# Kernel tuning notes

Hardware: AMD Instinct MI355X
Metric: run time of the kernel (lower is better)

The kernel has to match this reference:

```python
import jax, jax.numpy as jnp
import numpy as np

VQ_ALPHA = 0.5   # non-trainable vq_alpha weight, constant 0.5
BETA = 0.25      # commitment loss weight


def setup_inputs() -> dict:
    key = jax.random.key(0)
    k1, k2 = jax.random.split(key)
    x = jax.random.normal(k1, (16, 64, 64, 256), dtype=jnp.float32)
    # tf.keras RandomUniform default is U(-0.05, 0.05)
    dictionary = jax.random.uniform(k2, (256, 1024), dtype=jnp.float32,
                                    minval=-0.05, maxval=0.05)
    return {"x": x, "dictionary": dictionary}


def reference(x, dictionary):
    D, K = dictionary.shape  # embedding_dim, num_embeddings
    flat = x.reshape(-1, D)  # [N, D]

    # squared L2 distances: ||f||^2 + ||d||^2 - 2 f.d   -> [N, K]
    similarity = flat @ dictionary
    distances = (jnp.sum(flat * flat, axis=1, keepdims=True)
                 + jnp.sum(dictionary * dictionary, axis=0, keepdims=True)
                 - 2.0 * similarity)
    code_idx = jnp.argmin(distances, axis=1)  # [N]

    # one-hot @ dict^T is just a row gather of dict^T
    quantized = jnp.take(dictionary.T, code_idx, axis=0)  # [N, D]
    quantized = VQ_ALPHA * quantized
    q = quantized.reshape(x.shape)

    dictionary_loss = jnp.mean(jnp.square(jax.lax.stop_gradient(x) - q))
    commitment_loss = jnp.mean(jnp.square(x - jax.lax.stop_gradient(q)))
    loss = dictionary_loss + BETA * commitment_loss

    # straight-through estimator
    q_st = x + jax.lax.stop_gradient(q - x)
    return q_st, loss
```

## Files before the change

### kernel.cpp

```cpp
#include <hip/hip_runtime.h>


#define NROWS   65536
#define DIM     256
#define NCODE   1024
#define RPB     64
#define EPS_TIE 4e-3f

typedef _Float16 half8 __attribute__((ext_vector_type(8)));
typedef float    f32x4 __attribute__((ext_vector_type(4)));


__global__ void k_transpose(const float* __restrict__ dict, float* __restrict__ dictT) {
    int t = blockIdx.x * 256 + threadIdx.x;
#pragma unroll
    for (int i = 0; i < 4; ++i) {
        int e = i * 65536 + t;
        int d = e >> 10, k = e & 1023;
        dictT[k * DIM + d] = dict[e];
    }
}

__global__ void k_norms(const float* __restrict__ dict, float* __restrict__ dictnorm) {
    int k = blockIdx.x * 256 + threadIdx.x;
    float s = 0.f;
#pragma unroll 8
    for (int d = 0; d < DIM; ++d) {
        float v = dict[d * NCODE + k];
        s = fmaf(v, v, s);
    }
    dictnorm[k] = s;
}

__global__ void k_pack(const float* __restrict__ dict, unsigned short* __restrict__ packB) {
    int gid = blockIdx.x * 256 + threadIdx.x;
#pragma unroll
    for (int ii = 0; ii < 4; ++ii) {
        int o = ii * 65536 + gid;
        int j = o & 7, q = (o >> 3) & 3, n = (o >> 5) & 1023, kk = o >> 15;
        int d = kk * 32 + q * 8 + j;
        _Float16 h = (_Float16)dict[d * NCODE + n];
        packB[o] = *(unsigned short*)&h;
    }
}

__device__ __forceinline__ float np_pairwise_sq_128(const float* a, int stride) {
    float r[8];
#pragma unroll
    for (int j = 0; j < 8; ++j) {
        float v = a[j * stride];
        r[j] = __fmul_rn(v, v);
    }
    for (int i = 8; i < 128; i += 8) {
#pragma unroll
        for (int j = 0; j < 8; ++j) {
            float v = a[(i + j) * stride];
            r[j] = __fadd_rn(r[j], __fmul_rn(v, v));
        }
    }
    return __fadd_rn(__fadd_rn(__fadd_rn(r[0], r[1]), __fadd_rn(r[2], r[3])),
                     __fadd_rn(__fadd_rn(r[4], r[5]), __fadd_rn(r[6], r[7])));
}


__global__ __launch_bounds__(256, 4) void k_vq(
    const float* __restrict__ x, const float* __restrict__ dict,
    const float* __restrict__ dictT, const float* __restrict__ dictnorm,
    const unsigned short* __restrict__ packB,
    float* __restrict__ out, double* __restrict__ block_sums)
{
    __shared__ __align__(16) unsigned short bstage[8 * 2048];
    __shared__ float row_m1[RPB], row_m2[RPB];
    __shared__ int   row_k1[RPB], row_k2[RPB];
    __shared__ float red_d[256];
    __shared__ int   red_k[256];
    __shared__ float wred[4];
    __shared__ int   amb_list[RPB];
    __shared__ int   amb_cnt;

    const int tid  = threadIdx.x;
    const int ln   = tid & 63, wv = tid >> 6;
    const int l15  = ln & 15, q = ln >> 4;
    const int row0 = blockIdx.x * RPB;

    if (tid == 0) amb_cnt = 0;

    half8 afrag[8];
    {
        const float* ar = x + (size_t)(row0 + wv * 16 + l15) * DIM + q * 8;
#pragma unroll
        for (int kk = 0; kk < 8; ++kk) {
            const float4 p0 = *(const float4*)(ar + kk * 32);
            const float4 p1 = *(const float4*)(ar + kk * 32 + 4);
            half8 h;
            h[0] = (_Float16)p0.x; h[1] = (_Float16)p0.y; h[2] = (_Float16)p0.z; h[3] = (_Float16)p0.w;
            h[4] = (_Float16)p1.x; h[5] = (_Float16)p1.y; h[6] = (_Float16)p1.z; h[7] = (_Float16)p1.w;
            afrag[kk] = h;
        }
    }

    float m1[4], m2[4]; int j1[4], j2[4];
#pragma unroll
    for (int i = 0; i < 4; ++i) { m1[i] = 3.0e38f; m2[i] = 3.0e38f; j1[i] = 0x7fffffff; j2[i] = 0x7fffffff; }

    for (int cc = 0; cc < 16; ++cc) {
        const int c0 = cc * 64;
        __syncthreads();
        {
            const unsigned short* src = packB + (size_t)c0 * 32 + tid * 8;
            uint4 tmp[8];
#pragma unroll
            for (int kk = 0; kk < 8; ++kk) tmp[kk] = *(const uint4*)(src + (size_t)kk * 32768);
#pragma unroll
            for (int kk = 0; kk < 8; ++kk) *(uint4*)&bstage[kk * 2048 + tid * 8] = tmp[kk];
        }
        __syncthreads();

        float dn[4];
#pragma unroll
        for (int t = 0; t < 4; ++t) dn[t] = dictnorm[c0 + t * 16 + l15];

        const f32x4 zero = {0.f, 0.f, 0.f, 0.f};
        f32x4 acc[4];
#pragma unroll
        for (int t = 0; t < 4; ++t) acc[t] = zero;

#pragma unroll
        for (int kk = 0; kk < 8; ++kk) {
#pragma unroll
            for (int t = 0; t < 4; ++t) {
                const half8 b = *(const half8*)&bstage[kk * 2048 + (t * 16 + l15) * 32 + q * 8];
                acc[t] = __builtin_amdgcn_mfma_f32_16x16x32_f16(afrag[kk], b, acc[t], 0, 0, 0);
            }
        }

#pragma unroll
        for (int t = 0; t < 4; ++t) {
            const int k = c0 + t * 16 + l15;
#pragma unroll
            for (int i = 0; i < 4; ++i) {
                const float s = fmaf(-2.f, acc[t][i], dn[t]);
                if (s < m1[i])      { m2[i] = m1[i]; j2[i] = j1[i]; m1[i] = s; j1[i] = k; }
                else if (s < m2[i]) { m2[i] = s; j2[i] = k; }
            }
        }
    }

#pragma unroll
    for (int i = 0; i < 4; ++i) {
        float a1 = m1[i], a2 = m2[i]; int b1 = j1[i], b2 = j2[i];
#pragma unroll
        for (int sft = 1; sft < 16; sft <<= 1) {
            float o1 = __shfl_xor(a1, sft);
            float o2 = __shfl_xor(a2, sft);
            int   p1 = __shfl_xor(b1, sft);
            int   p2 = __shfl_xor(b2, sft);
            if (o1 < a1 || (o1 == a1 && p1 < b1)) {
                bool t = (a1 < o2) || (a1 == o2 && b1 < p2);
                a2 = t ? a1 : o2; b2 = t ? b1 : p2;
                a1 = o1; b1 = p1;
            } else {
                bool t = (o1 < a2) || (o1 == a2 && p1 < b2);
                a2 = t ? o1 : a2; b2 = t ? p1 : b2;
            }
        }
        if (l15 == 0) {
            const int r = wv * 16 + q * 4 + i;
            row_m1[r] = a1; row_m2[r] = a2; row_k1[r] = b1; row_k2[r] = b2;
        }
    }
    __syncthreads();

    if (tid < RPB && (row_m2[tid] - row_m1[tid]) < EPS_TIE) {
        int p = atomicAdd(&amb_cnt, 1);
        amb_list[p] = tid;
    }
    __syncthreads();
    const int namb = amb_cnt;

    for (int a = 0; a < namb; ++a) {
        const int r = amb_list[a];
        const float* xr = x + (size_t)(row0 + r) * DIM;
        const float nf = __fadd_rn(np_pairwise_sq_128(xr, 1), np_pairwise_sq_128(xr + 128, 1));
        float bd = 3.4e38f; int bk = 0x7fffffff;
#pragma unroll
        for (int i = 0; i < 4; ++i) {
            const int k = i * 256 + tid;
            float sim = 0.f, nd = 0.f;
            for (int d = 0; d < DIM; ++d) {
                const float dv = dict[(size_t)d * NCODE + k];
                const float fv = xr[d];
                sim = fmaf(fv, dv, sim);
                nd  = __fadd_rn(nd, __fmul_rn(dv, dv));
            }
            const float dist = __fsub_rn(__fadd_rn(nf, nd), __fmul_rn(2.f, sim));
            if (dist < bd) { bd = dist; bk = k; }
        }
        red_d[tid] = bd; red_k[tid] = bk;
        __syncthreads();
        for (int s = 128; s > 0; s >>= 1) {
            if (tid < s) {
                const float od = red_d[tid + s]; const int ok = red_k[tid + s];
                if (od < red_d[tid] || (od == red_d[tid] && ok < red_k[tid])) {
                    red_d[tid] = od; red_k[tid] = ok;
                }
            }
            __syncthreads();
        }
        if (tid == 0) row_k1[r] = red_k[0];
        __syncthreads();
    }

    float lsum = 0.f;
#pragma unroll 2
    for (int i = 0; i < 16; ++i) {
        const int e = i * 1024 + tid * 4;
        const int r = e >> 8, d0 = e & 255;
        const int kk = row_k1[r];
        const float4 dv = *(const float4*)&dictT[(size_t)kk * DIM + d0];
        const float4 xv = *(const float4*)&x[(size_t)row0 * DIM + e];
        float4 qv; qv.x = 0.5f * dv.x; qv.y = 0.5f * dv.y; qv.z = 0.5f * dv.z; qv.w = 0.5f * dv.w;
        float4 ov;
        ov.x = __fadd_rn(xv.x, __fsub_rn(qv.x, xv.x));
        ov.y = __fadd_rn(xv.y, __fsub_rn(qv.y, xv.y));
        ov.z = __fadd_rn(xv.z, __fsub_rn(qv.z, xv.z));
        ov.w = __fadd_rn(xv.w, __fsub_rn(qv.w, xv.w));
        const float e0 = __fsub_rn(xv.x, qv.x), e1 = __fsub_rn(xv.y, qv.y);
        const float e2 = __fsub_rn(xv.z, qv.z), e3 = __fsub_rn(xv.w, qv.w);
        lsum += e0 * e0 + e1 * e1 + e2 * e2 + e3 * e3;
        *(float4*)&out[(size_t)row0 * DIM + e] = ov;
    }

#pragma unroll
    for (int sft = 32; sft > 0; sft >>= 1) lsum += __shfl_down(lsum, sft, 64);
    if ((tid & 63) == 0) wred[tid >> 6] = lsum;
    __syncthreads();
    if (tid == 0)
        block_sums[blockIdx.x] = (double)((wred[0] + wred[1]) + (wred[2] + wred[3]));
}


__global__ void k_finalize(const double* __restrict__ block_sums, float* __restrict__ out_loss) {
    __shared__ double w[16];
    const int t = threadIdx.x;
    double v = block_sums[t];
#pragma unroll
    for (int sft = 32; sft > 0; sft >>= 1) v += __shfl_down(v, sft, 64);
    if ((t & 63) == 0) w[t >> 6] = v;
    __syncthreads();
    if (t == 0) {
        double tot = 0.0;
        for (int i = 0; i < 16; ++i) tot += w[i];
        out_loss[0] = (float)(1.25 * tot / (double)(NROWS * DIM));
    }
}


extern "C" void kernel_launch(void* const* d_in, const int* in_sizes, int n_in,
                              void* d_out, int out_size, void* d_ws, size_t ws_size,
                              hipStream_t stream) {
    (void)in_sizes; (void)n_in; (void)out_size; (void)ws_size;
    const float* x    = (const float*)d_in[0];
    const float* dict = (const float*)d_in[1];
    float* out = (float*)d_out;

    char* ws = (char*)d_ws;
    float*          dictT      = (float*)ws;
    float*          dictnorm   = (float*)(ws + 1048576);
    double*         block_sums = (double*)(ws + 1048576 + 4096);
    unsigned short* packB      = (unsigned short*)(ws + 1048576 + 4096 + 8192);

    k_transpose<<<256, 256, 0, stream>>>(dict, dictT);
    k_norms<<<4, 256, 0, stream>>>(dict, dictnorm);
    k_pack<<<256, 256, 0, stream>>>(dict, packB);
    k_vq<<<NROWS / RPB, 256, 0, stream>>>(x, dict, dictT, dictnorm, packB, out, block_sums);
    k_finalize<<<1, 1024, 0, stream>>>(block_sums, out + (size_t)NROWS * DIM);
}
```

Before: 305.8 us.

## Double-buffer codebook via async LDS loads, 128 rows per block, packed argmin

Merges the three dictionary prep kernels into one and doubles rows per block to 128, so each wave computes two 16-row MFMA tiles that share every B fragment loaded from LDS. Codebook tiles are staged with global_load_lds into a double buffer, letting the next chunk load while the current one is multiplied, which removes one barrier per chunk. The top-2 tracking packs a truncated distance and the code index into one unsigned key, so the running min and the shuffle reduction become integer min/max. The distance offset of +8 keeps the keys positive so integer ordering matches float ordering. The cost is a wider tie threshold to absorb the truncation, higher register and LDS use, and occupancy reduced to 2 blocks per CU.

```diff
diff --git a/kernel.cpp b/kernel.cpp
--- a/kernel.cpp
+++ b/kernel.cpp
@@ -4,43 +4,34 @@
 #define NROWS   65536
 #define DIM     256
 #define NCODE   1024
-#define RPB     64
-#define EPS_TIE 4e-3f
+#define RPB     128
+#define NBLK    (NROWS / RPB)
+#define EPS_TIE 6e-3f
 
 typedef _Float16 half8 __attribute__((ext_vector_type(8)));
 typedef float    f32x4 __attribute__((ext_vector_type(4)));
 
-
-__global__ void k_transpose(const float* __restrict__ dict, float* __restrict__ dictT) {
-    int t = blockIdx.x * 256 + threadIdx.x;
-#pragma unroll
-    for (int i = 0; i < 4; ++i) {
-        int e = i * 65536 + t;
-        int d = e >> 10, k = e & 1023;
-        dictT[k * DIM + d] = dict[e];
-    }
-}
-
-__global__ void k_norms(const float* __restrict__ dict, float* __restrict__ dictnorm) {
-    int k = blockIdx.x * 256 + threadIdx.x;
-    float s = 0.f;
-#pragma unroll 8
-    for (int d = 0; d < DIM; ++d) {
-        float v = dict[d * NCODE + k];
-        s = fmaf(v, v, s);
-    }
-    dictnorm[k] = s;
-}
-
-__global__ void k_pack(const float* __restrict__ dict, unsigned short* __restrict__ packB) {
+__global__ void k_prep(const float* __restrict__ dict, float* __restrict__ dictT,
+                       float* __restrict__ dictnorm, unsigned short* __restrict__ packB) {
     int gid = blockIdx.x * 256 + threadIdx.x;
 #pragma unroll
     for (int ii = 0; ii < 4; ++ii) {
         int o = ii * 65536 + gid;
-        int j = o & 7, q = (o >> 3) & 3, n = (o >> 5) & 1023, kk = o >> 15;
-        int d = kk * 32 + q * 8 + j;
-        _Float16 h = (_Float16)dict[d * NCODE + n];
-        packB[o] = *(unsigned short*)&h;
+        { int d = o >> 10, k = o & 1023; dictT[k * DIM + d] = dict[o]; }
+        { int j = o & 7, q = (o >> 3) & 3, n = (o >> 5) & 1023, kk = o >> 15;
+          int d = kk * 32 + q * 8 + j;
+          _Float16 h = (_Float16)dict[d * NCODE + n];
+          packB[o] = *(unsigned short*)&h; }
+    }
+    if (blockIdx.x < 4) {
+        int k = blockIdx.x * 256 + threadIdx.x;
+        float s = 0.f;
+#pragma unroll 8
+        for (int d = 0; d < DIM; ++d) {
+            float v = dict[d * NCODE + k];
+            s = fmaf(v, v, s);
+        }
+        dictnorm[k] = s + 8.0f;
     }
 }
 
@@ -63,15 +54,28 @@
 }
 
 
-__global__ __launch_bounds__(256, 4) void k_vq(
+#define STAGE(buf, cc) do {                                                            \
+    const int _t = tid >> 6, _q = (tid >> 4) & 3, _n = tid & 15;                       \
+    const unsigned short* _s = packB + (size_t)(cc) * 2048                             \
+                             + ((_t * 16 + _n) * 32 + _q * 8);                         \
+    unsigned short* _d = &bstage[buf][tid * 8];                                        \
+    _Pragma("unroll")                                                                  \
+    for (int _k = 0; _k < 8; ++_k)                                                     \
+        __builtin_amdgcn_global_load_lds(                                              \
+            (const __attribute__((address_space(1))) unsigned int*)(_s + (size_t)_k * 32768), \
+            (__attribute__((address_space(3))) unsigned int*)(_d + _k * 2048),         \
+            16, 0, 0);                                                                 \
+} while (0)
+
+__global__ __launch_bounds__(256, 2) void k_vq(
     const float* __restrict__ x, const float* __restrict__ dict,
     const float* __restrict__ dictT, const float* __restrict__ dictnorm,
     const unsigned short* __restrict__ packB,
     float* __restrict__ out, double* __restrict__ block_sums)
 {
-    __shared__ __align__(16) unsigned short bstage[8 * 2048];
-    __shared__ float row_m1[RPB], row_m2[RPB];
-    __shared__ int   row_k1[RPB], row_k2[RPB];
+    __shared__ __align__(16) unsigned short bstage[2][8 * 2048];
+    __shared__ float row_gap[RPB];
+    __shared__ int   row_k1[RPB];
     __shared__ float red_d[256];
     __shared__ int   red_k[256];
     __shared__ float wred[4];
@@ -82,12 +86,15 @@
     const int ln   = tid & 63, wv = tid >> 6;
     const int l15  = ln & 15, q = ln >> 4;
     const int row0 = blockIdx.x * RPB;
-
+    const int wrow = row0 + wv * 32;
+
+    STAGE(0, 0);
     if (tid == 0) amb_cnt = 0;
 
-    half8 afrag[8];
-    {
-        const float* ar = x + (size_t)(row0 + wv * 16 + l15) * DIM + q * 8;
+    half8 afrag[2][8];
+#pragma unroll
+    for (int u = 0; u < 2; ++u) {
+        const float* ar = x + (size_t)(wrow + u * 16 + l15) * DIM + q * 8;
 #pragma unroll
         for (int kk = 0; kk < 8; ++kk) {
             const float4 p0 = *(const float4*)(ar + kk * 32);
@@ -95,83 +102,84 @@
             half8 h;
             h[0] = (_Float16)p0.x; h[1] = (_Float16)p0.y; h[2] = (_Float16)p0.z; h[3] = (_Float16)p0.w;
             h[4] = (_Float16)p1.x; h[5] = (_Float16)p1.y; h[6] = (_Float16)p1.z; h[7] = (_Float16)p1.w;
-            afrag[kk] = h;
-        }
-    }
-
-    float m1[4], m2[4]; int j1[4], j2[4];
-#pragma unroll
-    for (int i = 0; i < 4; ++i) { m1[i] = 3.0e38f; m2[i] = 3.0e38f; j1[i] = 0x7fffffff; j2[i] = 0x7fffffff; }
+            afrag[u][kk] = h;
+        }
+    }
+
+    unsigned p1v[2][4], p2v[2][4];
+#pragma unroll
+    for (int u = 0; u < 2; ++u)
+#pragma unroll
+        for (int i = 0; i < 4; ++i) { p1v[u][i] = 0xFFFFFFFFu; p2v[u][i] = 0xFFFFFFFFu; }
+
+    __syncthreads();
 
     for (int cc = 0; cc < 16; ++cc) {
+        const int cur = cc & 1;
+        if (cc < 15) STAGE(cur ^ 1, cc + 1);
+
         const int c0 = cc * 64;
+        float dn[4];
+#pragma unroll
+        for (int t = 0; t < 4; ++t) dn[t] = dictnorm[c0 + t * 16 + l15];
+
+        const f32x4 zero = {0.f, 0.f, 0.f, 0.f};
+        f32x4 acc[2][4];
+#pragma unroll
+        for (int u = 0; u < 2; ++u)
+#pragma unroll
+            for (int t = 0; t < 4; ++t) acc[u][t] = zero;
+
+#pragma unroll
+        for (int kk = 0; kk < 8; ++kk) {
+#pragma unroll
+            for (int t = 0; t < 4; ++t) {
+                const half8 b = *(const half8*)&bstage[cur][kk * 2048 + t * 512 + ln * 8];
+                acc[0][t] = __builtin_amdgcn_mfma_f32_16x16x32_f16(afrag[0][kk], b, acc[0][t], 0, 0, 0);
+                acc[1][t] = __builtin_amdgcn_mfma_f32_16x16x32_f16(afrag[1][kk], b, acc[1][t], 0, 0, 0);
+            }
+        }
+
+#pragma unroll
+        for (int t = 0; t < 4; ++t) {
+            const unsigned kbase = (unsigned)(c0 + t * 16 + l15);
+#pragma unroll
+            for (int u = 0; u < 2; ++u)
+#pragma unroll
+                for (int i = 0; i < 4; ++i) {
+                    const float s = fmaf(-2.f, acc[u][t][i], dn[t]);
+                    const unsigned pk = (__float_as_uint(s) & 0xFFFFFC00u) | kbase;
+                    const unsigned mx = p1v[u][i] > pk ? p1v[u][i] : pk;
+                    p2v[u][i] = p2v[u][i] < mx ? p2v[u][i] : mx;
+                    p1v[u][i] = p1v[u][i] < pk ? p1v[u][i] : pk;
+                }
+        }
         __syncthreads();
-        {
-            const unsigned short* src = packB + (size_t)c0 * 32 + tid * 8;
-            uint4 tmp[8];
-#pragma unroll
-            for (int kk = 0; kk < 8; ++kk) tmp[kk] = *(const uint4*)(src + (size_t)kk * 32768);
-#pragma unroll
-            for (int kk = 0; kk < 8; ++kk) *(uint4*)&bstage[kk * 2048 + tid * 8] = tmp[kk];
-        }
-        __syncthreads();
-
-        float dn[4];
-#pragma unroll
-        for (int t = 0; t < 4; ++t) dn[t] = dictnorm[c0 + t * 16 + l15];
-
-        const f32x4 zero = {0.f, 0.f, 0.f, 0.f};
-        f32x4 acc[4];
-#pragma unroll
-        for (int t = 0; t < 4; ++t) acc[t] = zero;
-
-#pragma unroll
-        for (int kk = 0; kk < 8; ++kk) {
-#pragma unroll
-            for (int t = 0; t < 4; ++t) {
-                const half8 b = *(const half8*)&bstage[kk * 2048 + (t * 16 + l15) * 32 + q * 8];
-                acc[t] = __builtin_amdgcn_mfma_f32_16x16x32_f16(afrag[kk], b, acc[t], 0, 0, 0);
-            }
-        }
-
-#pragma unroll
-        for (int t = 0; t < 4; ++t) {
-            const int k = c0 + t * 16 + l15;
-#pragma unroll
-            for (int i = 0; i < 4; ++i) {
-                const float s = fmaf(-2.f, acc[t][i], dn[t]);
-                if (s < m1[i])      { m2[i] = m1[i]; j2[i] = j1[i]; m1[i] = s; j1[i] = k; }
-                else if (s < m2[i]) { m2[i] = s; j2[i] = k; }
-            }
-        }
-    }
-
-#pragma unroll
-    for (int i = 0; i < 4; ++i) {
-        float a1 = m1[i], a2 = m2[i]; int b1 = j1[i], b2 = j2[i];
-#pragma unroll
-        for (int sft = 1; sft < 16; sft <<= 1) {
-            float o1 = __shfl_xor(a1, sft);
-            float o2 = __shfl_xor(a2, sft);
-            int   p1 = __shfl_xor(b1, sft);
-            int   p2 = __shfl_xor(b2, sft);
-            if (o1 < a1 || (o1 == a1 && p1 < b1)) {
-                bool t = (a1 < o2) || (a1 == o2 && b1 < p2);
-                a2 = t ? a1 : o2; b2 = t ? b1 : p2;
-                a1 = o1; b1 = p1;
-            } else {
-                bool t = (o1 < a2) || (o1 == a2 && p1 < b2);
-                a2 = t ? o1 : a2; b2 = t ? p1 : b2;
-            }
-        }
-        if (l15 == 0) {
-            const int r = wv * 16 + q * 4 + i;
-            row_m1[r] = a1; row_m2[r] = a2; row_k1[r] = b1; row_k2[r] = b2;
-        }
-    }
-    __syncthreads();
-
-    if (tid < RPB && (row_m2[tid] - row_m1[tid]) < EPS_TIE) {
+    }
+
+#pragma unroll
+    for (int u = 0; u < 2; ++u)
+#pragma unroll
+        for (int i = 0; i < 4; ++i) {
+            unsigned a1 = p1v[u][i], a2 = p2v[u][i];
+#pragma unroll
+            for (int m = 1; m < 16; m <<= 1) {
+                const unsigned o1 = __shfl_xor(a1, m);
+                const unsigned o2 = __shfl_xor(a2, m);
+                const unsigned mx = a1 > o1 ? a1 : o1;
+                a1 = a1 < o1 ? a1 : o1;
+                const unsigned mn2 = a2 < o2 ? a2 : o2;
+                a2 = mx < mn2 ? mx : mn2;
+            }
+            if (l15 == 0) {
+                const int r = wv * 32 + u * 16 + q * 4 + i;
+                row_k1[r]  = (int)(a1 & 1023u);
+                row_gap[r] = __uint_as_float(a2 & 0xFFFFFC00u) - __uint_as_float(a1 & 0xFFFFFC00u);
+            }
+        }
+    __syncthreads();
+
+    if (tid < RPB && row_gap[tid] < EPS_TIE) {
         int p = atomicAdd(&amb_cnt, 1);
         amb_list[p] = tid;
     }
@@ -213,7 +221,7 @@
 
     float lsum = 0.f;
 #pragma unroll 2
-    for (int i = 0; i < 16; ++i) {
+    for (int i = 0; i < 32; ++i) {
         const int e = i * 1024 + tid * 4;
         const int r = e >> 8, d0 = e & 255;
         const int kk = row_k1[r];
@@ -241,7 +249,7 @@
 
 
 __global__ void k_finalize(const double* __restrict__ block_sums, float* __restrict__ out_loss) {
-    __shared__ double w[16];
+    __shared__ double w[8];
     const int t = threadIdx.x;
     double v = block_sums[t];
 #pragma unroll
@@ -250,7 +258,7 @@
     __syncthreads();
     if (t == 0) {
         double tot = 0.0;
-        for (int i = 0; i < 16; ++i) tot += w[i];
+        for (int i = 0; i < 8; ++i) tot += w[i];
         out_loss[0] = (float)(1.25 * tot / (double)(NROWS * DIM));
     }
 }
@@ -270,9 +278,7 @@
     double*         block_sums = (double*)(ws + 1048576 + 4096);
     unsigned short* packB      = (unsigned short*)(ws + 1048576 + 4096 + 8192);
 
-    k_transpose<<<256, 256, 0, stream>>>(dict, dictT);
-    k_norms<<<4, 256, 0, stream>>>(dict, dictnorm);
-    k_pack<<<256, 256, 0, stream>>>(dict, packB);
-    k_vq<<<NROWS / RPB, 256, 0, stream>>>(x, dict, dictT, dictnorm, packB, out, block_sums);
-    k_finalize<<<1, 1024, 0, stream>>>(block_sums, out + (size_t)NROWS * DIM);
-}
+    k_prep<<<256, 256, 0, stream>>>(dict, dictT, dictnorm, packB);
+    k_vq<<<NBLK, 256, 0, stream>>>(x, dict, dictT, dictnorm, packB, out, block_sums);
+    k_finalize<<<1, NBLK, 0, stream>>>(block_sums, out + (size_t)NROWS * DIM);
+}
```

Result: slower. 418.0 us (+36.7%).
